# Kernel tuning notes

Hardware: AMD Instinct MI355X
Metric: run time of the kernel (lower is better)

## Reference

```python
import math
import jax, jax.numpy as jnp
from jax import lax
import numpy as np

N_IMG = 2
C = 128
IMG_H, IMG_W = 512, 1024
STRIDES = (4, 8, 16, 32, 64)
SIZES = (32.0, 64.0, 128.0, 256.0, 512.0)
RATIOS = (0.5, 1.0, 2.0)
A = len(RATIOS)
PRE_NMS_TOPK = 2000    # pre_nms_topk[self.training] with training=True
POST_NMS_TOPK = 1000   # post_nms_topk[self.training]
NMS_THRESH = 0.7
BATCH_PER_IMG = 256
POS_FRAC = 0.5
MIN_BOX_SIZE = 0.0
SCALE_CLAMP = math.log(1000.0 / 16.0)
MATCH_LOW, MATCH_HIGH = 0.3, 0.7


def cell_anchors(size):
    rs = jnp.asarray(RATIOS, jnp.float32)
    area = size * size
    w = jnp.sqrt(area / rs)
    h = w * rs
    return jnp.stack([-w / 2, -h / 2, w / 2, h / 2], axis=1)  # [A,4]


def level_anchors(H, W, stride, size):
    ca = cell_anchors(size)
    sx = jnp.arange(W, dtype=jnp.float32) * stride
    sy = jnp.arange(H, dtype=jnp.float32) * stride
    yy, xx = jnp.meshgrid(sy, sx, indexing="ij")
    shifts = jnp.stack([xx, yy, xx, yy], axis=-1).reshape(-1, 4)  # [H*W,4]
    return (shifts[:, None, :] + ca[None, :, :]).reshape(-1, 4)  # [H*W*A,4]


def pairwise_iou(a, b):
    lt = jnp.maximum(a[:, None, :2], b[None, :, :2])
    rb = jnp.minimum(a[:, None, 2:], b[None, :, 2:])
    wh = jnp.clip(rb - lt, 0.0)
    inter = wh[..., 0] * wh[..., 1]
    area_a = (a[:, 2] - a[:, 0]) * (a[:, 3] - a[:, 1])
    area_b = (b[:, 2] - b[:, 0]) * (b[:, 3] - b[:, 1])
    union = area_a[:, None] + area_b[None, :] - inter
    return jnp.where(inter > 0, inter / union, 0.0)


def get_deltas(src, tgt):
    sw = src[..., 2] - src[..., 0]; sh = src[..., 3] - src[..., 1]
    scx = src[..., 0] + 0.5 * sw;   scy = src[..., 1] + 0.5 * sh
    tw = tgt[..., 2] - tgt[..., 0]; th = tgt[..., 3] - tgt[..., 1]
    tcx = tgt[..., 0] + 0.5 * tw;   tcy = tgt[..., 1] + 0.5 * th
    return jnp.stack([(tcx - scx) / sw, (tcy - scy) / sh,
                      jnp.log(tw / sw), jnp.log(th / sh)], axis=-1)


def apply_deltas(deltas, boxes):
    w = boxes[..., 2] - boxes[..., 0]; h = boxes[..., 3] - boxes[..., 1]
    cx = boxes[..., 0] + 0.5 * w;      cy = boxes[..., 1] + 0.5 * h
    dx, dy = deltas[..., 0], deltas[..., 1]
    dw = jnp.minimum(deltas[..., 2], SCALE_CLAMP)
    dh = jnp.minimum(deltas[..., 3], SCALE_CLAMP)
    pcx = dx * w + cx; pcy = dy * h + cy
    pw = jnp.exp(dw) * w; ph = jnp.exp(dh) * h
    return jnp.stack([pcx - 0.5 * pw, pcy - 0.5 * ph,
                      pcx + 0.5 * pw, pcy + 0.5 * ph], axis=-1)


def conv(x, w, b):
    y = lax.conv_general_dilated(x, w, (1, 1), "SAME",
                                 dimension_numbers=("NCHW", "OIHW", "NCHW"))
    return y + b[None, :, None, None]


def rpn_forward_flat(feats, conv_w, conv_b, obj_w, obj_b, delta_w, delta_b):
    anchors, logits, deltas = [], [], []
    for (stride, size), f in zip(zip(STRIDES, SIZES), feats):
        N, _, H, W = f.shape
        h = jax.nn.relu(conv(f, conv_w, conv_b))
        lg = conv(h, obj_w, obj_b)       # [N,A,H,W]
        dl = conv(h, delta_w, delta_b)   # [N,4A,H,W]
        logits.append(lg.transpose(0, 2, 3, 1).reshape(N, -1))                     # [N,HWA]
        deltas.append(dl.reshape(N, A, 4, H, W).transpose(0, 3, 4, 1, 2).reshape(N, -1, 4))
        anchors.append(level_anchors(H, W, stride, size))
    return anchors, logits, deltas


def label_and_sample(gt_b, key, anchors_all):
    iou = pairwise_iou(gt_b, anchors_all)                 # [G,R]
    matched_idxs = jnp.argmax(iou, axis=0)
    matched_vals = jnp.max(iou, axis=0)
    labels = jnp.where(matched_vals >= MATCH_HIGH, 1,
             jnp.where(matched_vals >= MATCH_LOW, -1, 0))
    highest = jnp.max(iou, axis=1)                        # per-gt best IoU
    lq = jnp.any((iou == highest[:, None]) & (highest[:, None] > 0), axis=0)
    labels = jnp.where(lq, 1, labels)                     # allow_low_quality_matches
    R = labels.shape[0]
    kf, kb = jax.random.split(key)
    fg = labels == 1; bg = labels == 0
    num_fg = jnp.minimum(fg.sum(), int(POS_FRAC * BATCH_PER_IMG))
    num_bg = jnp.minimum(bg.sum(), BATCH_PER_IMG - num_fg)
    def pick(mask, k, num):
        pri = jnp.where(mask, jax.random.uniform(k, (R,)), jnp.inf)
        rank = jnp.argsort(jnp.argsort(pri))
        return rank < num
    sel_fg = pick(fg, kf, num_fg)
    sel_bg = pick(bg, kb, num_bg)
    labels = jnp.where(sel_fg, 1, jnp.where(sel_bg, 0, -1))
    return labels, gt_b[matched_idxs]


def losses_fn(anchors_all, logits_cat, deltas_cat, gt_labels, matched_gt):
    fg = (gt_labels == 1).astype(logits_cat.dtype)          # [N,R]
    gt_deltas = get_deltas(anchors_all[None], matched_gt)   # [N,R,4]
    loc = jnp.sum(jnp.abs(deltas_cat - gt_deltas) * fg[..., None])  # smooth_l1, beta=0
    valid = (gt_labels >= 0).astype(logits_cat.dtype)
    x = logits_cat
    bce = jnp.maximum(x, 0.0) - x * fg + jnp.log1p(jnp.exp(-jnp.abs(x)))
    cls = jnp.sum(bce * valid)
    norm = float(BATCH_PER_IMG) * logits_cat.shape[0]
    return jnp.stack([cls / norm, loc / norm])


def nms_keep(boxes, valid):
    # boxes are sorted by descending score; greedy suppression.
    K = boxes.shape[0]
    iou = pairwise_iou(boxes, boxes)
    idx = jnp.arange(K)
    def body(i, keep):
        sup = (iou[i] > NMS_THRESH) & (idx > i) & keep[i]
        return keep & ~sup
    return lax.fori_loop(0, K, body, valid)


def predict_proposals(anchors, logits, deltas):
    lvl_boxes, lvl_scores = [], []
    for anc, lg, dl in zip(anchors, logits, deltas):
        boxes = apply_deltas(dl, anc[None])             # [N,R_l,4]
        k = min(PRE_NMS_TOPK, lg.shape[1])
        ts, ti = lax.top_k(lg, k)                       # [N,k]
        tb = jnp.take_along_axis(boxes, ti[..., None], axis=1)
        tb = jnp.stack([jnp.clip(tb[..., 0], 0.0, IMG_W), jnp.clip(tb[..., 1], 0.0, IMG_H),
                        jnp.clip(tb[..., 2], 0.0, IMG_W), jnp.clip(tb[..., 3], 0.0, IMG_H)], -1)
        valid = ((tb[..., 2] - tb[..., 0]) > MIN_BOX_SIZE) & ((tb[..., 3] - tb[..., 1]) > MIN_BOX_SIZE)
        keep = jax.vmap(nms_keep)(tb, valid)
        lvl_boxes.append(tb)
        lvl_scores.append(jnp.where(keep, ts, -jnp.inf))
    all_b = jnp.concatenate(lvl_boxes, axis=1)
    all_s = jnp.concatenate(lvl_scores, axis=1)
    fs, fi = lax.top_k(all_s, POST_NMS_TOPK)
    fb = jnp.take_along_axis(all_b, fi[..., None], axis=1)
    return fb, fs


def setup_inputs() -> dict:
    key = jax.random.key(0)
    ks = jax.random.split(key, 12)
    out = {}
    for i, s in enumerate(STRIDES):
        out[f"feat_p{i+2}"] = jax.random.normal(ks[i], (N_IMG, C, IMG_H // s, IMG_W // s), jnp.float32)
    G = 32
    wh_scale = jnp.asarray([IMG_W, IMG_H], jnp.float32)
    cxy = jax.random.uniform(ks[5], (N_IMG, G, 2)) * wh_scale
    wh = 32.0 + jax.random.uniform(ks[6], (N_IMG, G, 2)) * 224.0
    x1y1 = jnp.clip(cxy - wh / 2, 0.0)
    x2y2 = jnp.maximum(jnp.minimum(cxy + wh / 2, wh_scale), x1y1 + 1.0)
    out["gt_boxes"] = jnp.concatenate([x1y1, x2y2], axis=-1)
    out["conv_w"] = 0.01 * jax.random.normal(ks[7], (C, C, 3, 3), jnp.float32)
    out["conv_b"] = jnp.zeros((C,), jnp.float32)
    out["obj_w"] = 0.01 * jax.random.normal(ks[8], (A, C, 1, 1), jnp.float32)
    out["obj_b"] = jnp.zeros((A,), jnp.float32)
    out["delta_w"] = 0.01 * jax.random.normal(ks[9], (4 * A, C, 1, 1), jnp.float32)
    out["delta_b"] = jnp.zeros((4 * A,), jnp.float32)
    return out


def reference(feat_p2, feat_p3, feat_p4, feat_p5, feat_p6, gt_boxes,
              conv_w, conv_b, obj_w, obj_b, delta_w, delta_b):
    feats = [feat_p2, feat_p3, feat_p4, feat_p5, feat_p6]
    anchors, logits, deltas = rpn_forward_flat(feats, conv_w, conv_b, obj_w, obj_b, delta_w, delta_b)
    anchors_all = jnp.concatenate(anchors, axis=0)      # [R,4]
    logits_cat = jnp.concatenate(logits, axis=1)        # [N,R]
    deltas_cat = jnp.concatenate(deltas, axis=1)        # [N,R,4]
    keys = jax.random.split(jax.random.key(42), gt_boxes.shape[0])
    gt_labels, matched_gt = jax.vmap(label_and_sample, in_axes=(0, 0, None))(gt_boxes, keys, anchors_all)
    losses = losses_fn(anchors_all, logits_cat, deltas_cat, gt_labels, matched_gt)
    prop_boxes, prop_scores = predict_proposals(
        anchors,
        [lax.stop_gradient(l) for l in logits],
        [lax.stop_gradient(d) for d in deltas])
    return prop_boxes, prop_scores, losses
```

## Files before the change

### kernel.cpp

```cpp
#include <hip/hip_runtime.h>
#include <stdint.h>
#include <math.h>


#define R_TOT   130944
#define HALF_R  65472
#define TOTK    7920
#define SCALE_CLAMP 4.135166556742356

__host__ __device__ inline void threefry(uint32_t k0, uint32_t k1,
                                         uint32_t x0, uint32_t x1,
                                         uint32_t* o0, uint32_t* o1)
{
  uint32_t ks[3]; ks[0]=k0; ks[1]=k1; ks[2]=k0^k1^0x1BD11BDAu;
  x0 += ks[0]; x1 += ks[1];
  const uint32_t rot0[4] = {13u,15u,26u,6u};
  const uint32_t rot1[4] = {17u,29u,16u,24u};
  for (int i = 0; i < 5; i++){
    const uint32_t* rot = (i & 1) ? rot1 : rot0;
    for (int q = 0; q < 4; q++){
      x0 += x1;
      x1 = (x1 << rot[q]) | (x1 >> (32u - rot[q]));
      x1 ^= x0;
    }
    x0 += ks[(i+1)%3];
    x1 += ks[(i+2)%3] + (uint32_t)(i+1);
  }
  *o0 = x0; *o1 = x1;
}

__device__ inline unsigned long long mono64(double v){
  unsigned long long b = (unsigned long long)__double_as_longlong(v);
  return (b & 0x8000000000000000ull) ? ~b : (b | 0x8000000000000000ull);
}

__device__ __forceinline__ double iou_cf(double g0,double g1,double g2,double g3,
                                         double a0,double a1,double a2,double a3){
  #pragma clang fp contract(off)
  double lt0 = fmax(g0,a0), lt1 = fmax(g1,a1);
  double rb0 = fmin(g2,a2), rb1 = fmin(g3,a3);
  double w = rb0-lt0; if (w<0.0) w=0.0;
  double h = rb1-lt1; if (h<0.0) h=0.0;
  double inter = w*h;
  double aa = (g2-g0)*(g3-g1);
  double ab = (a2-a0)*(a3-a1);
  double uni = aa+ab-inter;
  return inter>0.0 ? inter/uni : 0.0;
}

__device__ __forceinline__ void anchor_of(int r, double* o){
  #pragma clang fp contract(off)
  const int    base[5]={0,98304,122880,129024,130560};
  const int    Wl[5]  ={256,128,64,32,16};
  const double strd[5]={4.0,8.0,16.0,32.0,64.0};
  const double size[5]={32.0,64.0,128.0,256.0,512.0};
  const double ratio[3]={0.5,1.0,2.0};
  int l=0; while (l<4 && r>=base[l+1]) l++;
  int rr=r-base[l]; int pix=rr/3; int a=rr-pix*3;
  int x=pix%Wl[l], y=pix/Wl[l];
  double w=sqrt(size[l]*size[l]/ratio[a]);
  double h=w*ratio[a];
  double sx=(double)x*strd[l], sy=(double)y*strd[l];
  o[0]=sx-0.5*w; o[1]=sy-0.5*h; o[2]=sx+0.5*w; o[3]=sy+0.5*h;
}

__device__ __forceinline__ void decode_box(int ridx, const double* __restrict__ d,
                                           double* __restrict__ o){
  double a[4]; anchor_of(ridx,a);
  double w=a[2]-a[0], h=a[3]-a[1];
  double cx=a[0]+0.5*w, cy=a[1]+0.5*h;
  double dw=fmin(d[2],SCALE_CLAMP), dh=fmin(d[3],SCALE_CLAMP);
  double pcx=d[0]*w+cx, pcy=d[1]*h+cy;
  double pw=exp(dw)*w, ph=exp(dh)*h;
  double x1=pcx-0.5*pw, y1=pcy-0.5*ph;
  double x2=pcx+0.5*pw, y2=pcy+0.5*ph;
  o[0]=fmin(fmax(x1,0.0),1024.0); o[1]=fmin(fmax(y1,0.0),512.0);
  o[2]=fmin(fmax(x2,0.0),1024.0); o[3]=fmin(fmax(y2,0.0),512.0);
}

__device__ inline void bitonic_desc(double* sv, int* si, int M, int tid, int nthr){
  for (int k=2;k<=M;k<<=1)
    for (int j=k>>1;j>0;j>>=1){
      __syncthreads();
      for (int i=tid;i<M;i+=nthr){
        int ixj=i^j;
        if (ixj>i){
          double va=sv[i], vb=sv[ixj]; int ia=si[i], ib=si[ixj];
          bool before = (va>vb) || (va==vb && ia<ib);
          bool up = ((i&k)==0);
          if (up ? !before : before){ sv[i]=vb; sv[ixj]=va; si[i]=ib; si[ixj]=ia; }
        }
      }
    }
  __syncthreads();
}

__device__ inline void bitonic_asc_u(uint32_t* sk, int* si, int M, int tid, int nthr){
  for (int k=2;k<=M;k<<=1)
    for (int j=k>>1;j>0;j>>=1){
      __syncthreads();
      for (int i=tid;i<M;i+=nthr){
        int ixj=i^j;
        if (ixj>i){
          uint32_t ka=sk[i], kb=sk[ixj]; int ia=si[i], ib=si[ixj];
          bool before = (ka<kb) || (ka==kb && ia<ib);
          bool up = ((i&k)==0);
          if (up ? !before : before){ sk[i]=kb; sk[ixj]=ka; si[i]=ib; si[ixj]=ia; }
        }
      }
    }
  __syncthreads();
}

__device__ inline void hist_select(int* hist, int kneed, int tid,
                                   int* shb, int* shk){
  for (int off=1; off<256; off<<=1){
    int v=0;
    if (tid<256 && tid>=off) v=hist[tid-off];
    __syncthreads();
    if (tid<256) hist[tid]+=v;
    __syncthreads();
  }
  if (tid<256){
    int prev = tid ? hist[tid-1] : 0;
    if (prev < kneed && kneed <= hist[tid]){ *shb=tid; *shk=kneed-prev; }
    if (tid==255 && kneed > hist[255]){ *shb=255; *shk=kneed-hist[254]; }
  }
  __syncthreads();
}

__global__ __launch_bounds__(256) void k_pre(const float* __restrict__ cw,
    float* __restrict__ cwTf, const float* __restrict__ gt,
    unsigned long long* __restrict__ highest)
{
  const int bx=blockIdx.x, tid=threadIdx.x;
  if (bx < 576){
    int o = bx*256 + tid;
    if (o >= 147456) return;
    int cc = o & 127; int t = o >> 7;
    int k9 = t % 9;  int ci = t / 9;
    cwTf[(size_t)(ci*9+k9)*128 + cc] = cw[(size_t)cc*1152 + ci*9 + k9];
  } else {
    __shared__ double gts[128];
    __shared__ unsigned long long lmax[32];
    const int gb=bx-576;
    const int img=gb>>6, b=gb&63;
    if (tid<128) gts[tid]=(double)gt[img*128+tid];
    if (tid<32) lmax[tid]=0ull;
    __syncthreads();
    double gm[32];
    #pragma unroll
    for (int g=0;g<32;g++) gm[g]=0.0;
    for (int r=b*256+tid; r<R_TOT; r+=64*256){
      double a[4]; anchor_of(r,a);
      #pragma unroll
      for (int g=0;g<32;g++){
        double v=iou_cf(gts[g*4],gts[g*4+1],gts[g*4+2],gts[g*4+3],a[0],a[1],a[2],a[3]);
        gm[g]=fmax(gm[g],v);
      }
    }
    #pragma unroll
    for (int g=0;g<32;g++){
      double v=gm[g];
      #pragma unroll
      for (int off=1; off<64; off<<=1) v=fmax(v,__shfl_xor(v,off));
      if ((tid&63)==0) atomicMax(&lmax[g],(unsigned long long)__double_as_longlong(v));
    }
    __syncthreads();
    if (tid<32) atomicMax(&highest[img*32+tid], lmax[tid]);
  }
}

#define CTH 4
#define CTW 8

__global__ __launch_bounds__(256,3) void k_conv_label(
    const float* __restrict__ f2, const float* __restrict__ f3,
    const float* __restrict__ f4, const float* __restrict__ f5,
    const float* __restrict__ f6,
    const float* __restrict__ cwTf, const float* __restrict__ cb,
    const float* __restrict__ ow, const float* __restrict__ ob,
    const float* __restrict__ dwt, const float* __restrict__ dbt,
    double* __restrict__ logits, double* __restrict__ dpred,
    const float* __restrict__ gt, const unsigned long long* __restrict__ highest,
    int* __restrict__ prelab, int* __restrict__ matched,
    int* __restrict__ labels, int* __restrict__ counts,
    uint32_t* __restrict__ ub,
    uint32_t kf00,uint32_t kf01,uint32_t kb00,uint32_t kb01,
    uint32_t kf10,uint32_t kf11,uint32_t kb10,uint32_t kb11)
{
  __shared__ double fshd[4][6][12];
  __shared__ __align__(16) char ush[18432];
  float*  wshF = (float*)ush;
  double* hshp = (double*)ush;
  __shared__ float hw[15*128];
  __shared__ float hb[15];

  const int tid=threadIdx.x;

  if (blockIdx.x >= 3752){
    int j = (blockIdx.x-3752)*256 + tid;
    if (j >= 2*R_TOT) return;
    int slot = j / HALF_R; int t = j - slot*HALF_R;
    uint32_t k0,k1;
    if      (slot==0){k0=kf00;k1=kf01;}
    else if (slot==1){k0=kb00;k1=kb01;}
    else if (slot==2){k0=kf10;k1=kf11;}
    else             {k0=kb10;k1=kb11;}
    uint32_t o0,o1;
    threefry(k0,k1,(uint32_t)t,(uint32_t)(t+HALF_R),&o0,&o1);
    ub[(size_t)slot*R_TOT+t]=o0;
    ub[(size_t)slot*R_TOT+t+HALF_R]=o1;
    return;
  }

  if (blockIdx.x >= 2728){
    double* gts=(double*)ush;
    double* hg =(double*)(ush+1024);
    int* wfg=(int*)(ush+1280); int* wbg=(int*)(ush+1296);
    const int lb=blockIdx.x-2728;
    const int img=lb>>9, blk=lb&511;
    if (tid<128) gts[tid]=(double)gt[img*128+tid];
    if (tid<32)  hg[tid]=__longlong_as_double((long long)highest[img*32+tid]);
    __syncthreads();
    int r=blk*256+tid;
    const bool ok=(r<R_TOT);
    int lab=-1, bi=0;
    if (ok){
      double a[4]; anchor_of(r,a);
      double best=-1.0; bool lq=false;
      #pragma unroll
      for (int g=0;g<32;g++){
        double v=iou_cf(gts[g*4],gts[g*4+1],gts[g*4+2],gts[g*4+3],a[0],a[1],a[2],a[3]);
        if (v>best){ best=v; bi=g; }
        if (hg[g]>0.0 && v==hg[g]) lq=true;
      }
      lab = lq ? 1 : (best>=0.7 ? 1 : (best>=0.3 ? -1 : 0));
      prelab [(size_t)img*R_TOT+r]=lab;
      matched[(size_t)img*R_TOT+r]=bi;
      labels [(size_t)img*R_TOT+r]=-1;
    }
    unsigned long long bf=__ballot(ok && lab==1);
    unsigned long long bb=__ballot(ok && lab==0);
    const int wid=tid>>6, lane=tid&63;
    if (lane==0){ wfg[wid]=__popcll(bf); wbg[wid]=__popcll(bb); }
    __syncthreads();
    if (tid==0){
      int fcnt=wfg[0]+wfg[1]+wfg[2]+wfg[3];
      int bcnt=wbg[0]+wbg[1]+wbg[2]+wbg[3];
      if (fcnt) atomicAdd(&counts[img*2+0],fcnt);
      if (bcnt) atomicAdd(&counts[img*2+1],bcnt);
    }
    return;
  }

  const int cumt[6]={0,2048,2560,2688,2720,2728};
  const int Hs[5]={128,64,32,16,8}, Wl[5]={256,128,64,32,16};
  const int rbs[5]={0,98304,122880,129024,130560};
  const int lgx[5]={5,4,3,2,1};

  int bid=blockIdx.x;
  int lvl=0;
  while (lvl<4 && bid>=cumt[lvl+1]) lvl++;
  int t=bid-cumt[lvl];
  const int img=t&1; const int tt=t>>1;
  const int H=Hs[lvl], W=Wl[lvl], rbase=rbs[lvl];
  const int tx=tt&((1<<lgx[lvl])-1), ty=tt>>lgx[lvl];
  const int x0=tx*CTW, y0=ty*CTH;
  const float* f = lvl==0?f2: lvl==1?f3: lvl==2?f4: lvl==3?f5: f6;

  for (int i=tid;i<15*128;i+=256){
    int o=i>>7, c=i&127;
    hw[i]=(o<3)?ow[o*128+c]:dwt[(o-3)*128+c];
  }
  if (tid<15) hb[tid]=(tid<3)?ob[tid]:dbt[tid-3];

  const int c=tid&127, half=tid>>7;
  double acc[16];
  #pragma unroll
  for (int i=0;i<16;i++) acc[i]=0.0;

  const float* fimg = f + (size_t)img*128*H*W;

  const bool fin_act = (tid < 240);
  int ci_f=0,dy_f=0,dx_f=0; bool fin_valid=false;
  const float* fptr=fimg;
  if (fin_act){
    ci_f=tid/60; int rem=tid-ci_f*60; dy_f=rem/10; dx_f=rem-dy_f*10;
    int y=y0-1+dy_f, x=x0-1+dx_f;
    fin_valid = (y>=0&&y<H&&x>=0&&x<W);
    fptr = fimg + (size_t)ci_f*H*W + (fin_valid ? ((size_t)y*W+x) : 0);
  }
  const size_t fstep=(size_t)4*H*W;
  const float2* wsrc=(const float2*)cwTf;

  float fin_pf=0.f; float2 wpf[9];
  if (fin_act){ fin_pf = fin_valid ? *fptr : 0.f; fptr += fstep; }
  #pragma unroll
  for (int j2=0;j2<9;j2++) wpf[j2]=wsrc[tid+j2*256];

  for (int ci0=0; ci0<128; ci0+=4){
    __syncthreads();
    if (fin_act) fshd[ci_f][dy_f][dx_f]=(double)fin_pf;
    { float2* wdst=(float2*)wshF;
      #pragma unroll
      for (int j2=0;j2<9;j2++) wdst[tid+j2*256]=wpf[j2]; }
    if (ci0+4<128){
      if (fin_act){ fin_pf = fin_valid ? *fptr : 0.f; fptr += fstep; }
      const float2* wn = wsrc + (size_t)(ci0+4)*576;
      #pragma unroll
      for (int j2=0;j2<9;j2++) wpf[j2]=wn[tid+j2*256];
    }
    __syncthreads();
    #pragma unroll
    for (int ci=0;ci<4;ci++){
      double w9d[9];
      #pragma unroll
      for (int k=0;k<9;k++) w9d[k]=(double)wshF[(ci*9+k)*128 + c];
      #pragma unroll
      for (int irl=0;irl<4;irl++){
        int ir=half*2+irl;
        double rowb[10];
        #pragma unroll
        for (int q=0;q<10;q++) rowb[q]=fshd[ci][ir][q];
        #pragma unroll
        for (int orl=0;orl<2;orl++){
          int ky=irl-orl;
          if (ky<0||ky>2) continue;
          #pragma unroll
          for (int px=0;px<8;px++){
            double s=acc[orl*8+px];
            #pragma unroll
            for (int kx=0;kx<3;kx++) s += w9d[ky*3+kx]*rowb[px+kx];
            acc[orl*8+px]=s;
          }
        }
      }
    }
  }
  double bc=(double)cb[c];
  __syncthreads();
  if (half==0){
    #pragma unroll
    for (int pp=0;pp<16;pp++){
      double hv=acc[pp]+bc; if (hv<0.0) hv=0.0;
      hshp[c*17+pp]=hv;
    }
  }
  __syncthreads();
  for (int hp=0;hp<2;hp++){
    if (tid<240){
      int o=tid>>4, p=tid&15;
      double s=(double)hb[o];
      for (int c2=0;c2<128;c2++) s += (double)hw[o*128+c2]*hshp[c2*17+p];
      int pg=hp*16+p;
      int py=pg>>3, px=pg&7;
      int gy=y0+py, gx=x0+px;
      long long pix=(long long)gy*W+gx;
      size_t rb=(size_t)rbase+(size_t)pix*3;
      if (o<3) logits[(size_t)img*R_TOT+rb+o]=s;
      else { int a=(o-3)>>2, jj=(o-3)&3; dpred[((size_t)img*R_TOT+rb+a)*4+jj]=s; }
    }
    if (hp==0){
      __syncthreads();
      if (half==1){
        #pragma unroll
        for (int pp=0;pp<16;pp++){
          double hv=acc[pp]+bc; if (hv<0.0) hv=0.0;
          hshp[c*17+pp]=hv;
        }
      }
      __syncthreads();
    }
  }
}

__global__ __launch_bounds__(1024) void k_mid2(const uint32_t* __restrict__ ub,
    const int* __restrict__ prelab, const int* __restrict__ counts,
    int* __restrict__ labels,
    const double* __restrict__ logits, const double* __restrict__ dpred,
    double* __restrict__ allS, double* __restrict__ allB,
    unsigned long long* __restrict__ keepbuf)
{
  __shared__ __align__(16) char buf[49152];
  __shared__ int hist[256];
  __shared__ int sI0, sI1;
  __shared__ int cnt;
  const int tid=threadIdx.x;

  if (blockIdx.x < 4){
    uint32_t* skey=(uint32_t*)buf; int* sidx=(int*)(buf+16384);
    const int img=blockIdx.x>>1, cls=blockIdx.x&1;
    const int cfg=counts[img*2+0], cbg=counts[img*2+1];
    const int num_fg=cfg<128?cfg:128;
    const int cap_bg=256-num_fg;
    const int num=cls?(cbg<cap_bg?cbg:cap_bg):num_fg;
    if (num<=0) return;
    const int want=cls?0:1;
    const int sel=want;
    const uint32_t* u=ub+(size_t)(img*2+cls)*R_TOT;
    const int* pl=prelab+(size_t)img*R_TOT;
    int* lab=labels+(size_t)img*R_TOT;

    for (int b=tid;b<256;b+=1024) hist[b]=0;
    if (tid==0) cnt=0;
    __syncthreads();
    #pragma unroll 4
    for (int r=tid;r<R_TOT;r+=1024){
      int plr = pl[r];
      uint32_t key = u[r]>>9;
      if (plr==want) atomicAdd(&hist[key>>15],1);
    }
    __syncthreads();
    hist_select(hist, num, tid, &sI0, &sI1);
    const uint32_t bsel=(uint32_t)sI0; const int kneed=sI1;
    #pragma unroll 4
    for (int r=tid;r<R_TOT;r+=1024){
      int plr = pl[r];
      uint32_t key = u[r]>>9;
      if (plr==want){
        uint32_t t8=key>>15;
        if (t8<bsel) lab[r]=sel;
        else if (t8==bsel){ int p=atomicAdd(&cnt,1); if (p<4096){ skey[p]=key; sidx[p]=r; } }
      }
    }
    __syncthreads();
    int n=cnt<4096?cnt:4096;
    for (int i=tid;i<4096;i+=1024) if (i>=n){ skey[i]=0xFFFFFFFFu; sidx[i]=0x7FFFFFFF; }
    bitonic_asc_u(skey,sidx,4096,tid,1024);
    int take = kneed<n?kneed:n;
    for (int i=tid;i<take;i+=1024) lab[sidx[i]]=sel;
  } else {
    double* sv=(double*)buf; int* si=(int*)(buf+32768);
    const int Rl[5]   ={98304,24576,6144,1536,384};
    const int kl[5]   ={2000,2000,2000,1536,384};
    const int lbase[5]={0,98304,122880,129024,130560};
    const int loff[5] ={0,2000,4000,6000,7536};
    const int bb=blockIdx.x-4;
    const int lvl=bb%5, img=bb/5;
    if (lvl==0 && tid<124) keepbuf[img*124+tid]=~0ull;
    const int Rn=Rl[lvl], K=kl[lvl];
    const double* lg=logits+(size_t)img*R_TOT+lbase[lvl];

    unsigned long long chosen=0; int kneed=K;
    for (int ps=7; ps>=6; --ps){
      int shift=ps*8;
      for (int b=tid;b<256;b+=1024) hist[b]=0;
      __syncthreads();
      #pragma unroll 4
      for (int r=tid;r<Rn;r+=1024){
        unsigned long long ik=~mono64(lg[r]);
        bool okp=(ps==7)||((ik>>(shift+8))==(chosen>>(shift+8)));
        if (okp) atomicAdd(&hist[(int)((ik>>shift)&255)],1);
      }
      __syncthreads();
      hist_select(hist, kneed, tid, &sI0, &sI1);
      chosen = chosen | ((unsigned long long)sI0<<shift);
      kneed  = sI1;
      __syncthreads();
    }
    const unsigned long long lim = chosen | 0xFFFFFFFFFFFFull;
    if (tid==0) cnt=0;
    __syncthreads();
    #pragma unroll 4
    for (int r=tid;r<Rn;r+=1024){
      unsigned long long ik=~mono64(lg[r]);
      if (ik<=lim){ int p=atomicAdd(&cnt,1); if (p<4096){ sv[p]=lg[r]; si[p]=r; } }
    }
    __syncthreads();
    int n=cnt<4096?cnt:4096;
    for (int i=tid;i<4096;i+=1024) if (i>=n){ sv[i]=-HUGE_VAL; si[i]=0x7FFFFFFF; }
    bitonic_desc(sv,si,4096,tid,1024);
    for (int j=tid;j<K;j+=1024){
      double v=sv[j]; int r=si[j];
      size_t slot=(size_t)img*TOTK+loff[lvl]+j;
      allS[slot]=v;
      int ridx=lbase[lvl]+r;
      double bx[4];
      decode_box(ridx, dpred+((size_t)img*R_TOT+ridx)*4, bx);
      allB[slot*4+0]=bx[0]; allB[slot*4+1]=bx[1]; allB[slot*4+2]=bx[2]; allB[slot*4+3]=bx[3];
    }
  }
}

__global__ __launch_bounds__(256) void k_mid3(const double* __restrict__ allB,
    unsigned long long* __restrict__ msk,
    const double* __restrict__ logits, const double* __restrict__ dpred,
    const float* __restrict__ gt, const int* __restrict__ labels,
    const int* __restrict__ matched, double* __restrict__ part)
{
  const int bx=blockIdx.x, tid=threadIdx.x;
  if (bx < 1980){
    __shared__ double Bsh[8000];
    const int kl[5]  ={2000,2000,2000,1536,384};
    const int loff[5]={0,2000,4000,6000,7536};
    const int rbc[6] ={0,250,500,750,942,990};
    const int img = bx/990; int t = bx - img*990;
    int lvl=0; while (lvl<4 && t>=rbc[lvl+1]) lvl++;
    const int i0=(t-rbc[lvl])*8;
    const int K=kl[lvl]; const int nw=(K+63)>>6;
    const double* B=allB+(size_t)(img*TOTK+loff[lvl])*4;
    for (int q=tid;q<K*4;q+=256) Bsh[q]=B[q];
    __syncthreads();
    const int wv=tid>>6, lane=tid&63;
    for (int rr=0;rr<8;rr++){
      int i=i0+rr;
      if (i>=K) break;
      const double bi0=Bsh[i*4],bi1=Bsh[i*4+1],bi2=Bsh[i*4+2],bi3=Bsh[i*4+3];
      const double areai=(bi2-bi0)*(bi3-bi1);
      for (int w=wv;w<nw;w+=4){
        int j=w*64+lane;
        bool pred=false;
        if (j<K && j>i){
          double a0=Bsh[j*4],a1=Bsh[j*4+1],a2=Bsh[j*4+2],a3=Bsh[j*4+3];
          double lt0=fmax(bi0,a0), lt1=fmax(bi1,a1);
          double rb0=fmin(bi2,a2), rb1=fmin(bi3,a3);
          double ww=rb0-lt0; if (ww<0.0) ww=0.0;
          double hh=rb1-lt1; if (hh<0.0) hh=0.0;
          double inter=ww*hh;
          double uni=areai+(a2-a0)*(a3-a1)-inter;
          double iou=inter>0.0?inter/uni:0.0;
          pred = iou>0.7;
        }
        unsigned long long m=__ballot(pred);
        if (lane==0) msk[((size_t)img*TOTK+loff[lvl]+i)*32+w]=m;
      }
    }
  } else {
    const int bid2=bx-1980;
    double cls=0.0, loc=0.0;
    for (int idx=bid2*256+tid; idx<2*R_TOT; idx+=256*256){
      int l=labels[idx];
      if (l<0) continue;
      double x=logits[idx];
      double fgv=(l==1)?1.0:0.0;
      cls += fmax(x,0.0)-x*fgv+log1p(exp(-fabs(x)));
      if (l==1){
        int img=idx/R_TOT, r=idx-img*R_TOT;
        double a[4]; anchor_of(r,a);
        int m=matched[idx];
        const float* g=gt+img*128+m*4;
        double sw=a[2]-a[0], sh=a[3]-a[1];
        double scx=a[0]+0.5*sw, scy=a[1]+0.5*sh;
        double tw=(double)g[2]-(double)g[0], th=(double)g[3]-(double)g[1];
        double tcx=(double)g[0]+0.5*tw, tcy=(double)g[1]+0.5*th;
        double d0=(tcx-scx)/sw, d1=(tcy-scy)/sh;
        double d2=log(tw/sw), d3=log(th/sh);
        const double* dp=dpred+(size_t)idx*4;
        loc += fabs(dp[0]-d0)+fabs(dp[1]-d1)+fabs(dp[2]-d2)+fabs(dp[3]-d3);
      }
    }
    __shared__ double sc[256], sl[256];
    sc[tid]=cls; sl[tid]=loc; __syncthreads();
    for (int s=128;s>0;s>>=1){
      if (tid<s){ sc[tid]+=sc[tid+s]; sl[tid]+=sl[tid+s]; }
      __syncthreads();
    }
    if (tid==0){ part[bid2*2]=sc[0]; part[bid2*2+1]=sl[0]; }
  }
}

#define NMS_LD(BUF, BASE) do{ \
  _Pragma("unroll") \
  for (int j_=0;j_<16;j_++){ int i_=(BASE)+j_; \
    BUF[j_] = (lane<nw && i_<K) ? M[(size_t)i_*32+lane] : 0ull; } \
}while(0)
#define NMS_PR(BUF, BASE) do{ \
  _Pragma("unroll") \
  for (int j_=0;j_<16;j_++){ int i_=(BASE)+j_; \
    if (i_<K){ unsigned long long kw_=__shfl(keep,(i_>>6)); \
      if ((kw_>>(i_&63))&1ull) keep &= ~BUF[j_]; } } \
}while(0)

__global__ __launch_bounds__(1024) void k_post(const double* __restrict__ allB,
    const double* __restrict__ allS, const unsigned long long* __restrict__ msk,
    const double* __restrict__ part, int* __restrict__ flags,
    unsigned long long* __restrict__ keepbuf, float* __restrict__ out)
{
  const int tid=threadIdx.x, bx=blockIdx.x;
  const int kl[5]  ={2000,2000,2000,1536,384};
  const int loff[5]={0,2000,4000,6000,7536};

  if (bx < 10){
    if (tid >= 64) return;
    const int lvl=bx%5, img=bx/5;
    const int K=kl[lvl], off=loff[lvl], nw=(K+63)>>6;
    const int lane=tid;
    const double* B=allB+(size_t)(img*TOTK+off)*4;
    const unsigned long long* M=msk+((size_t)img*TOTK+off)*32;
    unsigned long long keep=0ull;
    if (lane<nw){
      for (int b=0;b<64;b++){
        int j=lane*64+b;
        if (j<K){
          double x1=B[(size_t)j*4],y1=B[(size_t)j*4+1],x2=B[(size_t)j*4+2],y2=B[(size_t)j*4+3];
          if ((x2-x1)>0.0 && (y2-y1)>0.0) keep|=(1ull<<b);
        }
      }
    }
    unsigned long long Abuf[16], Bbuf[16];
    NMS_LD(Abuf, 0);
    for (int base=0; base<K; base+=32){
      NMS_LD(Bbuf, base+16);
      NMS_PR(Abuf, base);
      NMS_LD(Abuf, base+32);
      NMS_PR(Bbuf, base+16);
    }
    if (lane<nw){
      int nvalid = K - lane*64; if (nvalid>64) nvalid=64;
      unsigned long long vm = (nvalid>=64) ? ~0ull : ((1ull<<nvalid)-1ull);
      unsigned long long cbits = (~keep) & vm;
      int gbase = off + lane*64;
      int w0 = gbase>>6, sh = gbase&63;
      unsigned long long* kb = keepbuf + (size_t)img*124;
      if (sh==0){
        if (cbits) atomicAnd(&kb[w0], ~cbits);
      } else {
        unsigned long long lo = cbits << sh;
        unsigned long long hi = cbits >> (64-sh);
        if (lo) atomicAnd(&kb[w0],   ~lo);
        if (hi) atomicAnd(&kb[w0+1], ~hi);
      }
    }
    __threadfence();
    if (tid==0) atomicAdd(&flags[img],1);
    return;
  }

  if (bx < 12){
    const int img=bx-10;
    if (tid==0){
      while (atomicAdd(&flags[img],0) < 5) __builtin_amdgcn_s_sleep(8);
    }
    __syncthreads();
    __threadfence();
    __shared__ unsigned long long kbl[124];
    if (tid<124) kbl[tid]=atomicAdd(&keepbuf[(size_t)img*124+tid],0ull);
    __syncthreads();
    const double* sarr=allS+(size_t)img*TOTK;
    __shared__ int hist[256];
    __shared__ int sI0, sI1;
    __shared__ double sv[4096]; __shared__ int si[4096]; __shared__ int cnt;

    unsigned long long chosen=0; int kneed=1000;
    for (int ps=7; ps>=6; --ps){
      int shift=ps*8;
      for (int b=tid;b<256;b+=1024) hist[b]=0;
      __syncthreads();
      for (int r=tid;r<TOTK;r+=1024){
        bool kept = (kbl[r>>6]>>(r&63))&1ull;
        double val = kept ? sarr[r] : -HUGE_VAL;
        unsigned long long ik=~mono64(val);
        bool okp=(ps==7)||((ik>>(shift+8))==(chosen>>(shift+8)));
        if (okp) atomicAdd(&hist[(int)((ik>>shift)&255)],1);
      }
      __syncthreads();
      hist_select(hist, kneed, tid, &sI0, &sI1);
      chosen = chosen | ((unsigned long long)sI0<<shift);
      kneed  = sI1;
      __syncthreads();
    }
    const unsigned long long lim = chosen | 0xFFFFFFFFFFFFull;
    if (tid==0) cnt=0;
    __syncthreads();
    for (int r=tid;r<TOTK;r+=1024){
      bool kept = (kbl[r>>6]>>(r&63))&1ull;
      double val = kept ? sarr[r] : -HUGE_VAL;
      unsigned long long ik=~mono64(val);
      if (ik<=lim){ int p=atomicAdd(&cnt,1); if (p<4096){ sv[p]=val; si[p]=r; } }
    }
    __syncthreads();
    int n=cnt<4096?cnt:4096;
    for (int i=tid;i<4096;i+=1024) if (i>=n){ sv[i]=-HUGE_VAL; si[i]=0x7FFFFFFF; }
    bitonic_desc(sv,si,4096,tid,1024);
    for (int j=tid;j<1000;j+=1024){
      out[8000+img*1000+j]=(float)sv[j];
      int idx=si[j];
      const double* b=allB+((size_t)img*TOTK+idx)*4;
      float* ob=out+((size_t)img*1000+j)*4;
      ob[0]=(float)b[0]; ob[1]=(float)b[1]; ob[2]=(float)b[2]; ob[3]=(float)b[3];
    }
    return;
  }

  __shared__ double sc[256], sl[256];
  if (tid<256){ sc[tid]=part[tid*2]; sl[tid]=part[tid*2+1]; }
  __syncthreads();
  for (int s=128;s>0;s>>=1){
    if (tid<s){ sc[tid]+=sc[tid+s]; sl[tid]+=sl[tid+s]; }
    __syncthreads();
  }
  if (tid==0){ out[10000]=(float)(sc[0]/512.0); out[10001]=(float)(sl[0]/512.0); }
}

extern "C" void kernel_launch(void* const* d_in, const int* in_sizes, int n_in,
                              void* d_out, int out_size, void* d_ws, size_t ws_size,
                              hipStream_t stream)
{
  (void)in_sizes; (void)n_in; (void)out_size;
  const float* feats[5];
  for (int i=0;i<5;i++) feats[i]=(const float*)d_in[i];
  const float* gt =(const float*)d_in[5];
  const float* cw =(const float*)d_in[6];
  const float* cb =(const float*)d_in[7];
  const float* ow =(const float*)d_in[8];
  const float* ob =(const float*)d_in[9];
  const float* dwt=(const float*)d_in[10];
  const float* dbt=(const float*)d_in[11];
  float* out=(float*)d_out;

  char* p=(char*)d_ws;
  auto carve=[&](size_t nbytes)->char*{ char* q=p; p += (nbytes+255)&~(size_t)255; return q; };
  double* logits =(double*)carve(2ull*R_TOT*8);
  double* dpred  =(double*)carve(2ull*R_TOT*4*8);
  float* cwTf    =(float*)carve(147456ull*4);
  uint32_t* ub   =(uint32_t*)carve(4ull*R_TOT*4);
  int* prelab    =(int*)carve(2ull*R_TOT*4);
  int* matched   =(int*)carve(2ull*R_TOT*4);
  int* labels    =(int*)carve(2ull*R_TOT*4);
  unsigned long long* highest=(unsigned long long*)carve(2*32*8);
  int* counts    =(int*)carve(256);
  int* flags     =(int*)carve(256);
  double* allS   =(double*)carve(2ull*TOTK*8);
  double* allB   =(double*)carve(2ull*TOTK*4*8);
  unsigned long long* msk=(unsigned long long*)carve(2ull*TOTK*32*8);
  double* part   =(double*)carve(256*2*8);
  unsigned long long* keepbuf=(unsigned long long*)carve(2*124*8);
  if ((size_t)(p-(char*)d_ws) > ws_size) return;

  hipMemsetAsync(highest, 0, 1024, stream);

  uint32_t a0,b0,a1,b1;
  threefry(0u,42u,0u,2u,&a0,&b0);
  threefry(0u,42u,1u,3u,&a1,&b1);
  uint32_t kf00,kf01,kb00,kb01,kf10,kf11,kb10,kb11;
  { uint32_t c0,d0,c1,d1;
    threefry(a0,a1,0u,2u,&c0,&d0); threefry(a0,a1,1u,3u,&c1,&d1);
    kf00=c0; kf01=c1; kb00=d0; kb01=d1;
    threefry(b0,b1,0u,2u,&c0,&d0); threefry(b0,b1,1u,3u,&c1,&d1);
    kf10=c0; kf11=c1; kb10=d0; kb11=d1; }

  k_pre<<<704, 256, 0, stream>>>(cw, cwTf, gt, highest);
  k_conv_label<<<4775, 256, 0, stream>>>(feats[0],feats[1],feats[2],feats[3],feats[4],
      cwTf,cb,ow,ob,dwt,dbt, logits, dpred,
      gt, highest, prelab, matched, labels, counts,
      ub, kf00,kf01,kb00,kb01,kf10,kf11,kb10,kb11);
  k_mid2<<<14, 1024, 0, stream>>>(ub, prelab, counts, labels, logits, dpred, allS, allB, keepbuf);
  k_mid3<<<2236, 256, 0, stream>>>(allB, msk, logits, dpred, gt, labels, matched, part);
  k_post<<<13, 1024, 0, stream>>>(allB, allS, msk, part, flags, keepbuf, out);
}
```

Measured before the change: 1.343 ms.

## Restructure NMS suppression as per-word diagonal resolve plus masked OR of kept rows

Replaces the row-by-row NMS sweep, which prefetched mask rows in double buffers and did one shuffle and conditional AND per candidate, with a word-blocked scheme. For each 64-box word, the diagonal block is resolved inside the wavefront using shuffles. Each later lane then ORs in only the mask rows of boxes that were kept and ANDs that into its keep word. The aim is to skip mask loads for suppressed boxes and shorten the serial dependency chain, at the cost of data-dependent global loads inside the inner loop. A trivial blockIdx alias is also added.

```diff
diff --git a/kernel.cpp b/kernel.cpp
--- a/kernel.cpp
+++ b/kernel.cpp
@@ -197,9 +197,10 @@
   __shared__ float hb[15];
 
   const int tid=threadIdx.x;
-
-  if (blockIdx.x >= 3752){
-    int j = (blockIdx.x-3752)*256 + tid;
+  const int vbid = blockIdx.x;
+
+  if (vbid >= 3752){
+    int j = (vbid-3752)*256 + tid;
     if (j >= 2*R_TOT) return;
     int slot = j / HALF_R; int t = j - slot*HALF_R;
     uint32_t k0,k1;
@@ -214,11 +215,11 @@
     return;
   }
 
-  if (blockIdx.x >= 2728){
+  if (vbid >= 2728){
     double* gts=(double*)ush;
     double* hg =(double*)(ush+1024);
     int* wfg=(int*)(ush+1280); int* wbg=(int*)(ush+1296);
-    const int lb=blockIdx.x-2728;
+    const int lb=vbid-2728;
     const int img=lb>>9, blk=lb&511;
     if (tid<128) gts[tid]=(double)gt[img*128+tid];
     if (tid<32)  hg[tid]=__longlong_as_double((long long)highest[img*32+tid]);
@@ -259,7 +260,7 @@
   const int rbs[5]={0,98304,122880,129024,130560};
   const int lgx[5]={5,4,3,2,1};
 
-  int bid=blockIdx.x;
+  int bid=vbid;
   int lvl=0;
   while (lvl<4 && bid>=cumt[lvl+1]) lvl++;
   int t=bid-cumt[lvl];
@@ -560,18 +561,6 @@
   }
 }
 
-#define NMS_LD(BUF, BASE) do{ \
-  _Pragma("unroll") \
-  for (int j_=0;j_<16;j_++){ int i_=(BASE)+j_; \
-    BUF[j_] = (lane<nw && i_<K) ? M[(size_t)i_*32+lane] : 0ull; } \
-}while(0)
-#define NMS_PR(BUF, BASE) do{ \
-  _Pragma("unroll") \
-  for (int j_=0;j_<16;j_++){ int i_=(BASE)+j_; \
-    if (i_<K){ unsigned long long kw_=__shfl(keep,(i_>>6)); \
-      if ((kw_>>(i_&63))&1ull) keep &= ~BUF[j_]; } } \
-}while(0)
-
 __global__ __launch_bounds__(1024) void k_post(const double* __restrict__ allB,
     const double* __restrict__ allS, const unsigned long long* __restrict__ msk,
     const double* __restrict__ part, int* __restrict__ flags,
@@ -598,13 +587,25 @@
         }
       }
     }
-    unsigned long long Abuf[16], Bbuf[16];
-    NMS_LD(Abuf, 0);
-    for (int base=0; base<K; base+=32){
-      NMS_LD(Bbuf, base+16);
-      NMS_PR(Abuf, base);
-      NMS_LD(Abuf, base+32);
-      NMS_PR(Bbuf, base+16);
+    for (int w=0; w<nw; w++){
+      int row = w*64 + lane;
+      unsigned long long diag = (row<K) ? M[(size_t)row*32+w] : 0ull;
+      unsigned long long cur = __shfl(keep, w);
+      for (int b=0;b<64;b++){
+        if ((cur>>b)&1ull){
+          unsigned long long d=__shfl(diag,b);
+          cur &= ~d;
+        }
+      }
+      if (lane==w) keep=cur;
+      unsigned long long sup=0ull;
+      if (lane>w && lane<nw){
+        #pragma unroll 4
+        for (int b=0;b<64;b++){
+          if ((cur>>b)&1ull) sup |= M[(size_t)(w*64+b)*32+lane];
+        }
+      }
+      keep &= ~sup;
     }
     if (lane<nw){
       int nvalid = K - lane*64; if (nvalid>64) nvalid=64;
```

Result: slower. 1.392 ms (+3.6%).
